# Performance work log

Measured on AMD Instinct MI355X. Metric: run time of the kernel, lower is better.

Reference implementation:

```python
import jax, jax.numpy as jnp
import numpy as np

N_HEADS = 16


def setup_inputs() -> dict:
    key = jax.random.key(0)
    ks = jax.random.split(key, 4)
    B, S, D = 2, 2048, 1024
    x = jax.random.normal(ks[0], (B, S, D), dtype=jnp.float32)
    scale = 1.0 / np.sqrt(D)
    Wq = jax.random.normal(ks[1], (D, D), dtype=jnp.float32) * scale
    Wk = jax.random.normal(ks[2], (D, D), dtype=jnp.float32) * scale
    Wv = jax.random.normal(ks[3], (D, D), dtype=jnp.float32) * scale
    bq = jnp.zeros((D,), jnp.float32)
    bk = jnp.zeros((D,), jnp.float32)
    bv = jnp.zeros((D,), jnp.float32)
    return {"x": x, "Wq": Wq, "bq": bq, "Wk": Wk, "bk": bk, "Wv": Wv, "bv": bv}


def _split_heads(t, n_heads):
    B, S, D = t.shape
    return t.reshape(B, S, n_heads, D // n_heads).transpose(0, 2, 1, 3)  # [B,H,S,hd]


def reference(x, Wq, bq, Wk, bk, Wv, bv):
    H = N_HEADS
    Q = _split_heads(x @ Wq + bq, H)
    K = _split_heads(x @ Wk + bk, H)
    V = _split_heads(x @ Wv + bv, H)
    head_size = Q.shape[-1]
    scores = jnp.einsum("bhqd,bhkd->bhqk", Q, K) / jnp.sqrt(jnp.float32(head_size))
    probs = jax.nn.softmax(scores, axis=-1)  # dropout p=0.01 -> identity in eval
    out = jnp.einsum("bhqk,bhkd->bhqd", probs, V)
    B, _, S, hd = out.shape
    return out.transpose(0, 2, 1, 3).reshape(B, S, H * hd)
```

## Files before the change

kernel.cpp:

```cpp
#include <hip/hip_runtime.h>
#include <hip/hip_bf16.h>

typedef __bf16 bf16x8 __attribute__((ext_vector_type(8)));
typedef __bf16 bf16x4 __attribute__((ext_vector_type(4)));
typedef float f32x4 __attribute__((ext_vector_type(4)));
typedef unsigned u32x2 __attribute__((ext_vector_type(2)));
typedef unsigned u32x4 __attribute__((ext_vector_type(4)));

#define B_ 2
#define S_ 2048
#define D_ 1024
#define H_ 16
#define HD_ 64
#define NT_ (S_ / 64)

__device__ inline void load_lds16(const __bf16* g, __bf16* l) {
  __builtin_amdgcn_global_load_lds(
      (const __attribute__((address_space(1))) void*)g,
      (__attribute__((address_space(3))) void*)l, 16, 0, 0);
}

__global__ __launch_bounds__(256) void prep(
    const float* __restrict__ X,
    const float* __restrict__ Wq, const float* __restrict__ Wk,
    const float* __restrict__ Wv,
    __bf16* __restrict__ Xb, __bf16* __restrict__ WT)
{
  const int z = blockIdx.z, t = threadIdx.x;
  if (z == 3) {
    size_t base = ((size_t)(blockIdx.y * 16 + blockIdx.x)) * 16384 + t * 4;
#pragma unroll
    for (int i = 0; i < 16; ++i) {
      size_t idx = base + (size_t)i * 1024;
      f32x4 v = *(const f32x4*)(X + idx);
      __bf16 o[4];
#pragma unroll
      for (int j = 0; j < 4; ++j) o[j] = (__bf16)v[j];
      *(ulong1*)(Xb + idx) = *(ulong1*)o;
    }
    return;
  }
  const float* W = (z == 0) ? Wq : (z == 1) ? Wk : Wv;
  __bf16* WTz = WT + (size_t)z * D_ * D_;
  const int k0 = blockIdx.y * 64, n0 = blockIdx.x * 64;

  __shared__ __bf16 T[64 * 72];
  {
    int kl = t >> 2, cg = (t & 3) * 16;
    const float* wp = W + (size_t)(k0 + kl) * D_ + n0 + cg;
    bf16x8 a, b;
#pragma unroll
    for (int j = 0; j < 4; ++j) { a[j] = (__bf16)wp[j];     a[4 + j] = (__bf16)wp[4 + j]; }
#pragma unroll
    for (int j = 0; j < 4; ++j) { b[j] = (__bf16)wp[8 + j]; b[4 + j] = (__bf16)wp[12 + j]; }
    *(bf16x8*)(T + kl * 72 + cg) = a;
    *(bf16x8*)(T + kl * 72 + cg + 8) = b;
  }
  __syncthreads();
  {
    int nl = t >> 2, kc = (t & 3) * 16;
    bf16x8 a, b;
#pragma unroll
    for (int j = 0; j < 8; ++j) a[j] = T[(kc + j) * 72 + nl];
#pragma unroll
    for (int j = 0; j < 8; ++j) b[j] = T[(kc + 8 + j) * 72 + nl];
    __bf16* op = WTz + (size_t)(n0 + nl) * D_ + k0 + kc;
    *(bf16x8*)(op) = a;
    *(bf16x8*)(op + 8) = b;
  }
}

__global__ __launch_bounds__(256) void qkv_gemm(
    const __bf16* __restrict__ Xb, const __bf16* __restrict__ WT,
    const float* __restrict__ bq, const float* __restrict__ bk,
    const float* __restrict__ bv,
    __bf16* __restrict__ Qw, __bf16* __restrict__ Kw, __bf16* __restrict__ VTw)
{
  const int z = blockIdx.z;
  const __bf16* Wz = WT + (size_t)z * D_ * D_;
  const float* bias = (z == 0) ? bq : (z == 1) ? bk : bv;
  __bf16* outp = (z == 0) ? Qw : (z == 1) ? Kw : VTw;
  const float mult = (z == 0) ? 0.125f * 1.44269504088896f : 1.0f;

  const int tid  = threadIdx.x;
  const int wave = tid >> 6, lane = tid & 63, ln = lane & 15, quad = lane >> 4;
  const int m0 = blockIdx.y * 128, n0 = blockIdx.x * 128;
  const int wm = (wave & 1) * 64, wn = (wave >> 1) * 64;

  __shared__ __bf16 Als[128 * 32];
  __shared__ __bf16 Bls[128 * 32];

  f32x4 acc[4][4] = {};

  for (int k0 = 0; k0 < D_; k0 += 32) {
    __syncthreads();
#pragma unroll
    for (int i = 0; i < 2; ++i) {
      int cb = wave * 128 + i * 64;
      int chunk = cb + lane;
      int row = chunk >> 2, c = chunk & 3;
      int gc = c ^ (row & 3);
      load_lds16(Xb + (size_t)(m0 + row) * D_ + k0 + gc * 8, Als + cb * 8);
      load_lds16(Wz + (size_t)(n0 + row) * D_ + k0 + gc * 8, Bls + cb * 8);
    }
    __syncthreads();

    bf16x8 af[4], bfr[4];
    const int dsw = (quad ^ (ln & 3)) * 8;
#pragma unroll
    for (int mt = 0; mt < 4; ++mt)
      af[mt] = *(const bf16x8*)(Als + (wm + mt * 16 + ln) * 32 + dsw);
#pragma unroll
    for (int nt = 0; nt < 4; ++nt)
      bfr[nt] = *(const bf16x8*)(Bls + (wn + nt * 16 + ln) * 32 + dsw);
#pragma unroll
    for (int mt = 0; mt < 4; ++mt)
#pragma unroll
      for (int nt = 0; nt < 4; ++nt)
        acc[mt][nt] = __builtin_amdgcn_mfma_f32_16x16x32_bf16(af[mt], bfr[nt], acc[mt][nt], 0, 0, 0);
  }

#pragma unroll
  for (int nt = 0; nt < 4; ++nt) {
    int n_g = n0 + wn + nt * 16 + ln;
    float bv_ = bias[n_g];
#pragma unroll
    for (int mt = 0; mt < 4; ++mt) {
      if (z < 2) {
#pragma unroll
        for (int r = 0; r < 4; ++r) {
          int m_g = m0 + wm + mt * 16 + quad * 4 + r;
          outp[(size_t)m_g * D_ + n_g] = (__bf16)((acc[mt][nt][r] + bv_) * mult);
        }
      } else {
        int m_g0 = m0 + wm + mt * 16 + quad * 4;
        bf16x4 v4;
#pragma unroll
        for (int r = 0; r < 4; ++r) v4[r] = (__bf16)(acc[mt][nt][r] + bv_);
        *(bf16x4*)(outp + (size_t)(m_g0 >> 11) * D_ * S_ + (size_t)n_g * S_ + (m_g0 & (S_ - 1))) = v4;
      }
    }
  }
}

__global__ __launch_bounds__(256) void attn(
    const __bf16* __restrict__ Q, const __bf16* __restrict__ K,
    const __bf16* __restrict__ VT, float* __restrict__ out)
{
  const int tid  = threadIdx.x;
  const int wave = tid >> 6, lane = tid & 63, ln = lane & 15, quad = lane >> 4;

  const int f = blockIdx.x;
  const int xcd = f & 7, g = f >> 3;
  const int bh = ((g & 3) << 3) | xcd;
  const int qt = g >> 2;
  const int b = bh >> 4, h = bh & 15;
  const int q0 = qt * 128 + wave * 32;

  const __bf16* Qbase = Q + (size_t)(b * S_ + q0) * D_ + h * HD_;
  bf16x8 qb[2][2];
#pragma unroll
  for (int nt = 0; nt < 2; ++nt)
#pragma unroll
    for (int ks = 0; ks < 2; ++ks)
      qb[nt][ks] = *(const bf16x8*)(Qbase + (size_t)(nt * 16 + ln) * D_ + ks * 32 + quad * 8);

  const __bf16* Kh = K + (size_t)b * S_ * D_ + h * HD_;
  const __bf16* Vh = VT + (size_t)(b * D_ + h * HD_) * S_;

  __shared__ __bf16 Kls[2][64 * 64];
  __shared__ __bf16 Vls[2][64 * 64];

  bf16x8 vones;
#pragma unroll
  for (int j = 0; j < 8; ++j) vones[j] = (__bf16)1.0f;

  f32x4 acc[2][5] = {};
  const int swl = ln & 7;

  bf16x8 kreg[2], vreg[2];
#pragma unroll
  for (int i = 0; i < 2; ++i) {
    int chunk = i * 256 + tid, row = chunk >> 3, cc = chunk & 7;
    kreg[i] = *(const bf16x8*)(Kh + (size_t)row * D_ + cc * 8);
    vreg[i] = *(const bf16x8*)(Vh + (size_t)row * S_ + cc * 8);
  }

  bf16x8 vfrA[4][2], vfrB[4][2];
  bf16x8 paA[2][2], paB[2][2];

#define SLOT(KT_, VN, VP, PAN, PAP, DO_PV)                                     \
  {                                                                            \
    const int bi = (KT_) & 1;                                                  \
    __bf16* Kb = Kls[bi];                                                      \
    __bf16* Vb = Vls[bi];                                                      \
    _Pragma("unroll")                                                          \
    for (int i = 0; i < 2; ++i) {                                              \
      int chunk = i * 256 + tid, row = chunk >> 3, cc = chunk & 7;             \
      int sw = (cc ^ (row & 7)) * 8;                                           \
      *(bf16x8*)(Kb + row * 64 + sw) = kreg[i];                                \
      *(bf16x8*)(Vb + row * 64 + sw) = vreg[i];                                \
    }                                                                          \
    if ((KT_) + 1 < NT_) {                                                     \
      _Pragma("unroll")                                                        \
      for (int i = 0; i < 2; ++i) {                                            \
        int chunk = i * 256 + tid, row = chunk >> 3, cc = chunk & 7;           \
        kreg[i] = *(const bf16x8*)(Kh + (size_t)(((KT_) + 1) * 64 + row) * D_ + cc * 8); \
        vreg[i] = *(const bf16x8*)(Vh + (size_t)row * S_ + ((KT_) + 1) * 64 + cc * 8);   \
      }                                                                        \
    }                                                                          \
    __syncthreads();                                                           \
    _Pragma("unroll")                                                          \
    for (int dt = 0; dt < 4; ++dt)                                             \
      _Pragma("unroll")                                                        \
      for (int ks = 0; ks < 2; ++ks)                                           \
        VN[dt][ks] = *(const bf16x8*)(Vb + (dt * 16 + ln) * 64 + ((ks * 4 + quad) ^ swl) * 8); \
    f32x4 st[4][2] = {};                                                       \
    __builtin_amdgcn_s_setprio(1);                                             \
    _Pragma("unroll")                                                          \
    for (int mt = 0; mt < 4; ++mt)                                             \
      _Pragma("unroll")                                                        \
      for (int ks = 0; ks < 2; ++ks) {                                         \
        bf16x8 ka = *(const bf16x8*)(Kb + (mt * 16 + ln) * 64 + ((ks * 4 + quad) ^ swl) * 8); \
        _Pragma("unroll")                                                      \
        for (int nt = 0; nt < 2; ++nt)                                         \
          st[mt][nt] = __builtin_amdgcn_mfma_f32_16x16x32_bf16(ka, qb[nt][ks], st[mt][nt], 0, 0, 0); \
      }                                                                        \
    if (DO_PV) {                                                               \
      _Pragma("unroll")                                                        \
      for (int ks = 0; ks < 2; ++ks)                                           \
        _Pragma("unroll")                                                      \
        for (int dt = 0; dt < 5; ++dt) {                                       \
          bf16x8 vb = (dt < 4) ? VP[dt][ks] : vones;                           \
          _Pragma("unroll")                                                    \
          for (int nt = 0; nt < 2; ++nt)                                       \
            acc[nt][dt] = __builtin_amdgcn_mfma_f32_16x16x32_bf16(PAP[nt][ks], vb, acc[nt][dt], 0, 0, 0); \
        }                                                                      \
    }                                                                          \
    __builtin_amdgcn_s_setprio(0);                                             \
    _Pragma("unroll")                                                          \
    for (int nt = 0; nt < 2; ++nt)                                             \
      _Pragma("unroll")                                                        \
      for (int ks = 0; ks < 2; ++ks) {                                         \
        bf16x4 p0, p1;                                                         \
        _Pragma("unroll")                                                      \
        for (int r = 0; r < 4; ++r) {                                          \
          p0[r] = (__bf16)__builtin_amdgcn_exp2f(st[2 * ks + 0][nt][r]);       \
          p1[r] = (__bf16)__builtin_amdgcn_exp2f(st[2 * ks + 1][nt][r]);       \
        }                                                                      \
        u32x2 d0 = __builtin_bit_cast(u32x2, p0);                              \
        u32x2 d1 = __builtin_bit_cast(u32x2, p1);                              \
        unsigned a = d0[0], bw = d0[1], c = d1[0], e = d1[1];                  \
        asm("v_permlane32_swap_b32 %0, %1" : "+v"(a), "+v"(c));                \
        asm("v_permlane16_swap_b32 %0, %1" : "+v"(a), "+v"(c));                \
        asm("v_permlane32_swap_b32 %0, %1" : "+v"(bw), "+v"(e));               \
        asm("v_permlane16_swap_b32 %0, %1" : "+v"(bw), "+v"(e));               \
        u32x4 w;                                                               \
        w[0] = a; w[1] = bw; w[2] = c; w[3] = e;                               \
        PAN[nt][ks] = __builtin_bit_cast(bf16x8, w);                           \
      }                                                                        \
  }

  for (int kt = 0; kt < NT_; kt += 2) {
    SLOT(kt,     vfrA, vfrB, paA, paB, kt > 0);
    SLOT(kt + 1, vfrB, vfrA, paB, paA, 1);
  }
#undef SLOT

#pragma unroll
  for (int ks = 0; ks < 2; ++ks)
#pragma unroll
    for (int dt = 0; dt < 5; ++dt) {
      bf16x8 vb = (dt < 4) ? vfrB[dt][ks] : vones;
#pragma unroll
      for (int nt = 0; nt < 2; ++nt)
        acc[nt][dt] = __builtin_amdgcn_mfma_f32_16x16x32_bf16(paB[nt][ks], vb, acc[nt][dt], 0, 0, 0);
    }

#pragma unroll
  for (int nt = 0; nt < 2; ++nt)
#pragma unroll
    for (int r = 0; r < 4; ++r) {
      float li = 1.0f / acc[nt][4][r];
      float* op = out + (size_t)(b * S_ + q0 + nt * 16 + quad * 4 + r) * D_ + h * HD_;
#pragma unroll
      for (int dt = 0; dt < 4; ++dt)
        op[dt * 16 + ln] = acc[nt][dt][r] * li;
    }
}

extern "C" void kernel_launch(void* const* d_in, const int* in_sizes, int n_in,
                              void* d_out, int out_size, void* d_ws, size_t ws_size,
                              hipStream_t stream) {
  const float* X  = (const float*)d_in[0];
  const float* Wq = (const float*)d_in[1];
  const float* bq = (const float*)d_in[2];
  const float* Wk = (const float*)d_in[3];
  const float* bk = (const float*)d_in[4];
  const float* Wv = (const float*)d_in[5];
  const float* bv = (const float*)d_in[6];

  __bf16* Qw  = (__bf16*)d_ws;
  __bf16* Kw  = Qw  + (size_t)B_ * S_ * D_;
  __bf16* VTw = Kw  + (size_t)B_ * S_ * D_;
  __bf16* Xb  = VTw + (size_t)B_ * S_ * D_;
  __bf16* WT  = Xb  + (size_t)B_ * S_ * D_;
  float* out = (float*)d_out;

  prep<<<dim3(16, 16, 4), 256, 0, stream>>>(X, Wq, Wk, Wv, Xb, WT);
  qkv_gemm<<<dim3(8, 32, 3), 256, 0, stream>>>(Xb, WT, bq, bk, bv, Qw, Kw, VTw);
  attn<<<512, 256, 0, stream>>>(Qw, Kw, VTw, out);
}
```

Baseline: 158.6 us.

## Use direct global-to-LDS async loads for K/V tiles with double buffering

```diff
diff --git a/kernel.cpp b/kernel.cpp
--- a/kernel.cpp
+++ b/kernel.cpp
@@ -178,38 +178,25 @@
   f32x4 acc[2][5] = {};
   const int swl = ln & 7;
 
-  bf16x8 kreg[2], vreg[2];
-#pragma unroll
-  for (int i = 0; i < 2; ++i) {
-    int chunk = i * 256 + tid, row = chunk >> 3, cc = chunk & 7;
-    kreg[i] = *(const bf16x8*)(Kh + (size_t)row * D_ + cc * 8);
-    vreg[i] = *(const bf16x8*)(Vh + (size_t)row * S_ + cc * 8);
-  }
-
   bf16x8 vfrA[4][2], vfrB[4][2];
   bf16x8 paA[2][2], paB[2][2];
 
-#define SLOT(KT_, VN, VP, PAN, PAP, DO_PV)                                     \
+#define ISSUE_TILE(T_, BI_)                                                    \
   {                                                                            \
-    const int bi = (KT_) & 1;                                                  \
-    __bf16* Kb = Kls[bi];                                                      \
-    __bf16* Vb = Vls[bi];                                                      \
     _Pragma("unroll")                                                          \
     for (int i = 0; i < 2; ++i) {                                              \
-      int chunk = i * 256 + tid, row = chunk >> 3, cc = chunk & 7;             \
-      int sw = (cc ^ (row & 7)) * 8;                                           \
-      *(bf16x8*)(Kb + row * 64 + sw) = kreg[i];                                \
-      *(bf16x8*)(Vb + row * 64 + sw) = vreg[i];                                \
+      int cb = i * 256 + wave * 64;                                            \
+      int chunk = cb + lane, row = chunk >> 3, cc = chunk & 7;                 \
+      int gc = (cc ^ (row & 7)) * 8;            \
+      load_lds16(Kh + (size_t)((T_) * 64 + row) * D_ + gc, &Kls[BI_][cb * 8]); \
+      load_lds16(Vh + (size_t)row * S_ + (T_) * 64 + gc, &Vls[BI_][cb * 8]);   \
     }                                                                          \
-    if ((KT_) + 1 < NT_) {                                                     \
-      _Pragma("unroll")                                                        \
-      for (int i = 0; i < 2; ++i) {                                            \
-        int chunk = i * 256 + tid, row = chunk >> 3, cc = chunk & 7;           \
-        kreg[i] = *(const bf16x8*)(Kh + (size_t)(((KT_) + 1) * 64 + row) * D_ + cc * 8); \
-        vreg[i] = *(const bf16x8*)(Vh + (size_t)row * S_ + ((KT_) + 1) * 64 + cc * 8);   \
-      }                                                                        \
-    }                                                                          \
-    __syncthreads();                                                           \
+  }
+
+#define TILE(BI_, VN, VP, PAN, PAP, DO_PV)                                     \
+  {                                                                            \
+    const __bf16* Kb = Kls[BI_];                                               \
+    const __bf16* Vb = Vls[BI_];                                               \
     _Pragma("unroll")                                                          \
     for (int dt = 0; dt < 4; ++dt)                                             \
       _Pragma("unroll")                                                        \
@@ -261,11 +248,29 @@
       }                                                                        \
   }
 
+#define SYNC_PINNED()                                                          \
+  {                                                                            \
+    asm volatile("s_waitcnt vmcnt(0)" ::: "memory");                           \
+    __syncthreads();                                                           \
+    __builtin_amdgcn_sched_barrier(0);                                         \
+  }
+
+  ISSUE_TILE(0, 0);
+
   for (int kt = 0; kt < NT_; kt += 2) {
-    SLOT(kt,     vfrA, vfrB, paA, paB, kt > 0);
-    SLOT(kt + 1, vfrB, vfrA, paB, paA, 1);
-  }
-#undef SLOT
+    SYNC_PINNED();
+    ISSUE_TILE(kt + 1, 1);
+    __builtin_amdgcn_sched_barrier(0);
+    TILE(0, vfrA, vfrB, paA, paB, (kt > 0));
+
+    SYNC_PINNED();
+    if (kt + 2 < NT_) ISSUE_TILE(kt + 2, 0);
+    __builtin_amdgcn_sched_barrier(0);
+    TILE(1, vfrB, vfrA, paB, paA, 1);
+  }
+#undef TILE
+#undef ISSUE_TILE
+#undef SYNC_PINNED
 
 #pragma unroll
   for (int ks = 0; ks < 2; ++ks)
```

Result: no change. 158.3 us (-0.2%).
